# Kernel optimization log

Measured on AMD Instinct MI355X. Metric: run time of the kernel, lower is better.

## Reference

```python
import jax, jax.numpy as jnp
import numpy as np

S, B, C = 7, 2, 20
LAMBDA_COORD = 5.0
LAMBDA_NOOBJ = 0.5
WH_EPS = 1e-6
IOU_EPS = 1e-6
BATCH = 16384


def _iou_yolo(a, b):
    # a, b: [..., 4] in (cx, cy, w, h) 'yolo' center format
    ax1, ay1 = a[..., 0] - a[..., 2] / 2, a[..., 1] - a[..., 3] / 2
    ax2, ay2 = a[..., 0] + a[..., 2] / 2, a[..., 1] + a[..., 3] / 2
    bx1, by1 = b[..., 0] - b[..., 2] / 2, b[..., 1] - b[..., 3] / 2
    bx2, by2 = b[..., 0] + b[..., 2] / 2, b[..., 1] + b[..., 3] / 2
    iw = jnp.clip(jnp.minimum(ax2, bx2) - jnp.maximum(ax1, bx1), 0.0)
    ih = jnp.clip(jnp.minimum(ay2, by2) - jnp.maximum(ay1, by1), 0.0)
    inter = iw * ih
    area_a = jnp.abs((ax2 - ax1) * (ay2 - ay1))
    area_b = jnp.abs((bx2 - bx1) * (by2 - by1))
    return inter / (area_a + area_b - inter + IOU_EPS)


def setup_inputs() -> dict:
    key = jax.random.key(0)
    k1, k2, k3 = jax.random.split(key, 3)
    D = C + 5 * B  # 30
    y_trues = jax.random.uniform(k1, (BATCH, S, S, D), dtype=jnp.float32)
    # conf channel must be exactly 0.0 or 1.0 (loss branches on == 1)
    conf = (jax.random.uniform(k2, (BATCH, S, S)) < 0.3).astype(jnp.float32)
    y_trues = y_trues.at[..., 4].set(conf)
    y_preds = jax.random.normal(k3, (BATCH, S, S, D), dtype=jnp.float32)
    return {"y_trues": y_trues, "y_preds": y_preds}


def reference(y_trues, y_preds):
    D = C + 5 * B
    t = y_trues.reshape(-1, S * S, D)   # [N, 49, 30]
    p = y_preds.reshape(-1, S * S, D)
    batch_size = p.shape[0]

    b = t[..., 0:4]
    bhat1 = p[..., 0:4]
    bhat2 = p[..., 5:9]

    iou1 = _iou_yolo(b, bhat1)          # [N, 49]
    iou2 = _iou_yolo(b, bhat2)
    use1 = iou1 > iou2

    bhat = jnp.where(use1[..., None], bhat1, bhat2)            # responsible box
    confhat_chosen = jnp.where(use1, p[..., 4], p[..., 9])
    confhat_other = jnp.where(use1, p[..., 9], p[..., 4])

    # coord losses (object cells)
    xy = LAMBDA_COORD * ((b[..., 0] - bhat[..., 0]) ** 2 + (b[..., 1] - bhat[..., 1]) ** 2)
    wh = LAMBDA_COORD * (
        (jnp.sqrt(b[..., 2]) - jnp.sqrt(jnp.abs(bhat[..., 2] + WH_EPS))) ** 2
        + (jnp.sqrt(b[..., 3]) - jnp.sqrt(jnp.abs(bhat[..., 3] + WH_EPS))) ** 2
    )
    obj_conf = (t[..., 4] - confhat_chosen) ** 2
    noobj_in_obj = LAMBDA_NOOBJ * (0.0 - confhat_other) ** 2
    cls = jnp.sum((t[..., 10:] - p[..., 10:]) ** 2, axis=-1)

    obj_terms = xy + wh + obj_conf + noobj_in_obj + cls

    # no-object cells: penalize both predicted confs toward y_true conf (== target conf channel)
    noobj_terms = LAMBDA_NOOBJ * (
        (t[..., 4] - p[..., 4]) ** 2 + (t[..., 4] - p[..., 9]) ** 2
    )

    obj_mask = t[..., 4] == 1.0
    total = jnp.sum(jnp.where(obj_mask, obj_terms, noobj_terms))
    return total / batch_size
```

## Files before the change

### kernel.cpp

```cpp
#include <hip/hip_runtime.h>

#define LAMBDA_COORD 5.0f
#define LAMBDA_NOOBJ 0.5f
#define WH_EPS 1e-6f
#define IOU_EPS 1e-6f

constexpr int CHUNK_CELLS = 64;
constexpr int CHUNK_VEC4  = CHUNK_CELLS * 30/4;
constexpr int GRID        = 1280;

__device__ __forceinline__ float iou_yolo(float a0, float a1, float a2, float a3,
                                          float b0, float b1, float b2, float b3) {
    float ax1 = a0 - a2 * 0.5f, ay1 = a1 - a3 * 0.5f;
    float ax2 = a0 + a2 * 0.5f, ay2 = a1 + a3 * 0.5f;
    float bx1 = b0 - b2 * 0.5f, by1 = b1 - b3 * 0.5f;
    float bx2 = b0 + b2 * 0.5f, by2 = b1 + b3 * 0.5f;
    float iw = fmaxf(fminf(ax2, bx2) - fmaxf(ax1, bx1), 0.0f);
    float ih = fmaxf(fminf(ay2, by2) - fmaxf(ay1, by1), 0.0f);
    float inter = iw * ih;
    float area_a = fabsf((ax2 - ax1) * (ay2 - ay1));
    float area_b = fabsf((bx2 - bx1) * (by2 - by1));
    return inter / (area_a + area_b - inter + IOU_EPS);
}

__device__ __forceinline__ float cell_loss(const float* t, const float* p) {
    const float b0 = t[0], b1 = t[1], b2 = t[2], b3 = t[3], t4 = t[4];

    float iou1 = iou_yolo(b0, b1, b2, b3, p[0], p[1], p[2], p[3]);
    float iou2 = iou_yolo(b0, b1, b2, b3, p[5], p[6], p[7], p[8]);
    bool use1 = iou1 > iou2;

    float bh0 = use1 ? p[0] : p[5];
    float bh1 = use1 ? p[1] : p[6];
    float bh2 = use1 ? p[2] : p[7];
    float bh3 = use1 ? p[3] : p[8];
    float conf_c = use1 ? p[4] : p[9];
    float conf_o = use1 ? p[9] : p[4];

    float dx = b0 - bh0, dy = b1 - bh1;
    float xy = LAMBDA_COORD * (dx * dx + dy * dy);

    float sw = sqrtf(b2) - sqrtf(fabsf(bh2 + WH_EPS));
    float sh = sqrtf(b3) - sqrtf(fabsf(bh3 + WH_EPS));
    float wh = LAMBDA_COORD * (sw * sw + sh * sh);

    float dc = t4 - conf_c;
    float obj_conf = dc * dc;
    float noobj_in_obj = LAMBDA_NOOBJ * conf_o * conf_o;

    float cls = 0.0f;
#pragma unroll
    for (int k = 10; k < 30; ++k) {
        float d = t[k] - p[k];
        cls += d * d;
    }

    float obj_terms = xy + wh + obj_conf + noobj_in_obj + cls;

    float d4 = t4 - p[4], d9 = t4 - p[9];
    float noobj_terms = LAMBDA_NOOBJ * (d4 * d4 + d9 * d9);

    return (t4 == 1.0f) ? obj_terms : noobj_terms;
}

__device__ __forceinline__ void stage16(const float4* g_wave, float4* l_wave, int lane) {
    __builtin_amdgcn_global_load_lds(
        (const __attribute__((address_space(1))) void*)(g_wave + lane),
        (__attribute__((address_space(3))) void*)l_wave,
        16, 0, 0);
}

__device__ __forceinline__ void issue_array(const float4* g, float4* l, int lane) {
#pragma unroll
    for (int j = 0; j < 7; ++j)
        stage16(g + j * 64, l + j * 64, lane);
    if (lane < 32)
        stage16(g + 7 * 64, l + 7 * 64, lane);
}

__global__ __launch_bounds__(64) void yolo_loss_kernel(
    const float4* __restrict__ tv, const float4* __restrict__ pv,
    float* __restrict__ out, int nchunks, float inv_batch) {
    __shared__ float4 sbuf[2][2][CHUNK_VEC4];

    const int lane = threadIdx.x;

    float v = 0.0f;
    int g = blockIdx.x;
    int parity = 0;

    if (g < nchunks) {
        issue_array(tv + (size_t)g * CHUNK_VEC4, sbuf[0][0], lane);
        issue_array(pv + (size_t)g * CHUNK_VEC4, sbuf[0][1], lane);
    }

    while (g < nchunks) {
        const int gn = g + GRID;
        const bool have_next = gn < nchunks;
        if (have_next) {
            issue_array(tv + (size_t)gn * CHUNK_VEC4, sbuf[1 - parity][0], lane);
            issue_array(pv + (size_t)gn * CHUNK_VEC4, sbuf[1 - parity][1], lane);
            __builtin_amdgcn_s_waitcnt(0x4F70);
        } else {
            __builtin_amdgcn_s_waitcnt(0x0F70);
        }

        const float* st = (const float*)sbuf[parity][0];
        const float* sp = (const float*)sbuf[parity][1];
        v += cell_loss(st + lane * 30, sp + lane * 30);

        __builtin_amdgcn_s_waitcnt(0xC07F);

        parity = 1 - parity;
        g = gn;
    }

#pragma unroll
    for (int off = 32; off > 0; off >>= 1)
        v += __shfl_down(v, off, 64);

    if (lane == 0) atomicAdd(out, v * inv_batch);
}

extern "C" void kernel_launch(void* const* d_in, const int* in_sizes, int n_in,
                              void* d_out, int out_size, void* d_ws, size_t ws_size,
                              hipStream_t stream) {
    const float* t = (const float*)d_in[0];
    const float* p = (const float*)d_in[1];
    float* out = (float*)d_out;

    const int total = in_sizes[0];
    const int cells = total / 30;
    const int nchunks = cells / CHUNK_CELLS;
    const int batch = cells / 49;
    const float inv_batch = 1.0f / (float)batch;

    hipMemsetAsync(out, 0, sizeof(float), stream);

    yolo_loss_kernel<<<GRID, 64, 0, stream>>>(
        (const float4*)t, (const float4*)p, out, nchunks, inv_batch);
}
```

Baseline: 207.4 us.

## Replace LDS double-buffered staging with direct per-thread vector loads and two-pass reduction

Drops the 64-thread wavefront loop that staged chunks through LDS with global_load_lds double buffering. Each thread now loads two cells (15 float4) of targets and predictions straight into registers, with 256-thread blocks sized so each thread handles about two pairs. Per-block partials go to a workspace and a second single-block kernel reduces them, replacing the memset and atomics. The per-thread loads use a 240-byte stride, so accesses across a wave are strided and coalesce poorly. The 120 live floats per thread also raise register pressure and may limit occupancy.

```diff
diff --git a/kernel.cpp b/kernel.cpp
--- a/kernel.cpp
+++ b/kernel.cpp
@@ -5,9 +5,8 @@
 #define WH_EPS 1e-6f
 #define IOU_EPS 1e-6f
 
-constexpr int CHUNK_CELLS = 64;
-constexpr int CHUNK_VEC4  = CHUNK_CELLS * 30/4;
-constexpr int GRID        = 1280;
+
+constexpr int THREADS = 256;
 
 __device__ __forceinline__ float iou_yolo(float a0, float a1, float a2, float a3,
                                           float b0, float b1, float b2, float b3) {
@@ -63,63 +62,53 @@
     return (t4 == 1.0f) ? obj_terms : noobj_terms;
 }
 
-__device__ __forceinline__ void stage16(const float4* g_wave, float4* l_wave, int lane) {
-    __builtin_amdgcn_global_load_lds(
-        (const __attribute__((address_space(1))) void*)(g_wave + lane),
-        (__attribute__((address_space(3))) void*)l_wave,
-        16, 0, 0);
-}
+__global__ __launch_bounds__(THREADS, 3) void yolo_loss_main(
+    const float4* __restrict__ tv, const float4* __restrict__ pv,
+    float* __restrict__ ws, int npairs) {
+    const int stride = gridDim.x * THREADS;
+    float v = 0.0f;
 
-__device__ __forceinline__ void issue_array(const float4* g, float4* l, int lane) {
+    for (int pair = blockIdx.x * THREADS + threadIdx.x; pair < npairs; pair += stride) {
+        const float4* tg = tv + (size_t)pair * 15;
+        const float4* pg = pv + (size_t)pair * 15;
+        float4 tb[15], pb[15];
 #pragma unroll
-    for (int j = 0; j < 7; ++j)
-        stage16(g + j * 64, l + j * 64, lane);
-    if (lane < 32)
-        stage16(g + 7 * 64, l + 7 * 64, lane);
-}
-
-__global__ __launch_bounds__(64) void yolo_loss_kernel(
-    const float4* __restrict__ tv, const float4* __restrict__ pv,
-    float* __restrict__ out, int nchunks, float inv_batch) {
-    __shared__ float4 sbuf[2][2][CHUNK_VEC4];
-
-    const int lane = threadIdx.x;
-
-    float v = 0.0f;
-    int g = blockIdx.x;
-    int parity = 0;
-
-    if (g < nchunks) {
-        issue_array(tv + (size_t)g * CHUNK_VEC4, sbuf[0][0], lane);
-        issue_array(pv + (size_t)g * CHUNK_VEC4, sbuf[0][1], lane);
-    }
-
-    while (g < nchunks) {
-        const int gn = g + GRID;
-        const bool have_next = gn < nchunks;
-        if (have_next) {
-            issue_array(tv + (size_t)gn * CHUNK_VEC4, sbuf[1 - parity][0], lane);
-            issue_array(pv + (size_t)gn * CHUNK_VEC4, sbuf[1 - parity][1], lane);
-            __builtin_amdgcn_s_waitcnt(0x4F70);
-        } else {
-            __builtin_amdgcn_s_waitcnt(0x0F70);
-        }
-
-        const float* st = (const float*)sbuf[parity][0];
-        const float* sp = (const float*)sbuf[parity][1];
-        v += cell_loss(st + lane * 30, sp + lane * 30);
-
-        __builtin_amdgcn_s_waitcnt(0xC07F);
-
-        parity = 1 - parity;
-        g = gn;
+        for (int j = 0; j < 15; ++j) tb[j] = tg[j];
+#pragma unroll
+        for (int j = 0; j < 15; ++j) pb[j] = pg[j];
+        const float* tf = (const float*)tb;
+        const float* pf = (const float*)pb;
+        v += cell_loss(tf, pf) + cell_loss(tf + 30, pf + 30);
     }
 
 #pragma unroll
     for (int off = 32; off > 0; off >>= 1)
         v += __shfl_down(v, off, 64);
 
-    if (lane == 0) atomicAdd(out, v * inv_batch);
+    __shared__ float part[THREADS / 64];
+    if ((threadIdx.x & 63) == 0) part[threadIdx.x >> 6] = v;
+    __syncthreads();
+    if (threadIdx.x == 0) {
+        float s = 0.0f;
+#pragma unroll
+        for (int w = 0; w < THREADS / 64; ++w) s += part[w];
+        ws[blockIdx.x] = s;
+    }
+}
+
+__global__ __launch_bounds__(256) void yolo_loss_finish(
+    const float* __restrict__ ws, float* __restrict__ out,
+    int nblocks, float inv_batch) {
+    float v = 0.0f;
+    for (int i = threadIdx.x; i < nblocks; i += 256) v += ws[i];
+#pragma unroll
+    for (int off = 32; off > 0; off >>= 1)
+        v += __shfl_down(v, off, 64);
+    __shared__ float part[4];
+    if ((threadIdx.x & 63) == 0) part[threadIdx.x >> 6] = v;
+    __syncthreads();
+    if (threadIdx.x == 0)
+        out[0] = (part[0] + part[1] + part[2] + part[3]) * inv_batch;
 }
 
 extern "C" void kernel_launch(void* const* d_in, const int* in_sizes, int n_in,
@@ -128,15 +117,17 @@
     const float* t = (const float*)d_in[0];
     const float* p = (const float*)d_in[1];
     float* out = (float*)d_out;
+    float* ws = (float*)d_ws;
 
     const int total = in_sizes[0];
     const int cells = total / 30;
-    const int nchunks = cells / CHUNK_CELLS;
+    const int npairs = cells / 2;
     const int batch = cells / 49;
     const float inv_batch = 1.0f / (float)batch;
 
-    hipMemsetAsync(out, 0, sizeof(float), stream);
+    const int blocks = (npairs + THREADS * 2 - 1) / (THREADS * 2);
 
-    yolo_loss_kernel<<<GRID, 64, 0, stream>>>(
-        (const float4*)t, (const float4*)p, out, nchunks, inv_batch);
+    yolo_loss_main<<<blocks, THREADS, 0, stream>>>(
+        (const float4*)t, (const float4*)p, ws, npairs);
+    yolo_loss_finish<<<1, 256, 0, stream>>>(ws, out, blocks, inv_batch);
 }
```

Measured after the change: 216.2 us. 1.04x slower.
